# Kernel optimization log

Hardware: AMD Instinct MI355X
Metric: run time of the kernel (lower is better)

## Reference

```python
import jax, jax.numpy as jnp
import numpy as np

B, S, HID, H = 4, 2048, 1024, 16
D = HID // H  # dim per head


def setup_inputs() -> dict:
    key = jax.random.key(0)
    ks = jax.random.split(key, 7)
    inp = {
        "q": jax.random.normal(ks[0], (B, S, HID), dtype=jnp.float32),
        "k": jax.random.normal(ks[1], (B, S, HID), dtype=jnp.float32),
        "v": jax.random.normal(ks[2], (B, S, HID), dtype=jnp.float32),
        # Linear weights stored as (in, out); applied as x @ W. use_bias=False.
        "Wq": jax.random.normal(ks[3], (HID, HID), dtype=jnp.float32) * (1.0 / np.sqrt(HID)),
        "Wk": jax.random.normal(ks[4], (HID, HID), dtype=jnp.float32) * (1.0 / np.sqrt(HID)),
        "Wv": jax.random.normal(ks[5], (HID, HID), dtype=jnp.float32) * (1.0 / np.sqrt(HID)),
        "Wo": jax.random.normal(ks[6], (HID, HID), dtype=jnp.float32) * (1.0 / np.sqrt(HID)),
    }
    return inp


def reference(q, k, v, Wq, Wk, Wv, Wo):
    scale = 1.0 / jnp.sqrt(jnp.float32(D))
    # QKV projections, then split hidden into (H, D) heads (same layout as transpose_qkv)
    Q = (q @ Wq).reshape(B, S, H, D)
    K = (k @ Wk).reshape(B, S, H, D)
    V = (v @ Wv).reshape(B, S, H, D)
    # scaled dot-product attention: full [B,H,S,S] score matrix, softmax over keys
    attn_w = jnp.einsum("bqhd,bkhd->bhqk", Q, K) * scale
    attn_w = jax.nn.softmax(attn_w, axis=-1)
    # dropout rate is 0 (eval-mode / deterministic)
    O = jnp.einsum("bhqk,bkhd->bqhd", attn_w, V).reshape(B, S, HID)
    return O @ Wo
```

## Files before the change

### kernel.cpp

```cpp
#include <hip/hip_runtime.h>


typedef __attribute__((ext_vector_type(8))) short short8;
typedef __attribute__((ext_vector_type(4))) float float4v;

#if __has_builtin(__builtin_amdgcn_exp2f)
#define EXP2F(x) __builtin_amdgcn_exp2f(x)
#else
#define EXP2F(x) exp2f(x)
#endif

__device__ __forceinline__ unsigned short f2b(float x) {
  return (unsigned short)((__float_as_uint(x) + 0x8000u) >> 16);
}
__device__ __forceinline__ unsigned pk2f(float a, float b) {
  unsigned ua = __float_as_uint(a) + 0x8000u;
  unsigned ub = __float_as_uint(b) + 0x8000u;
  return __builtin_amdgcn_perm(ub, ua, 0x07060302);
}

typedef __attribute__((address_space(3))) unsigned int lds_uint;
typedef const __attribute__((address_space(1))) unsigned int gbl_uint;
__device__ __forceinline__ void stage16(const unsigned short* g, unsigned short* l) {
#if __has_builtin(__builtin_amdgcn_global_load_lds)
  __builtin_amdgcn_global_load_lds((gbl_uint*)g, (lds_uint*)l, 16, 0, 0);
#else
  *(uint4*)l = *(const uint4*)g;
#endif
}

__global__ __launch_bounds__(256) void conv_qkv(const float* __restrict__ q,
                                                const float* __restrict__ k,
                                                const float* __restrict__ v,
                                                unsigned short* __restrict__ ws,
                                                float qscale) {
  const int z = blockIdx.y;
  const float* src = z == 0 ? q : (z == 1 ? k : v);
  unsigned short* dst = ws + (size_t)z * 8388608;
  const float s = z == 0 ? qscale : 1.0f;
  size_t i = ((size_t)blockIdx.x * 256 + threadIdx.x) * 8;
  float4v a = *(const float4v*)(src + i);
  float4v b = *(const float4v*)(src + i + 4);
  uint4 o;
  o.x = pk2f(a.x * s, a.y * s);
  o.y = pk2f(a.z * s, a.w * s);
  o.z = pk2f(b.x * s, b.y * s);
  o.w = pk2f(b.z * s, b.w * s);
  *(uint4*)(dst + i) = o;
}

__global__ __launch_bounds__(256) void wtrans(const float* __restrict__ Wq,
                                              const float* __restrict__ Wk,
                                              const float* __restrict__ Wv,
                                              const float* __restrict__ Wo,
                                              unsigned short* __restrict__ Wt) {
  __shared__ float tile[32][33];
  const float* W = blockIdx.z == 0 ? Wq : blockIdx.z == 1 ? Wk
                   : blockIdx.z == 2 ? Wv : Wo;
  unsigned short* T = Wt + (size_t)blockIdx.z * 1048576;
  const int tx = threadIdx.x & 31, ty = threadIdx.x >> 5;
  const int k0 = blockIdx.y * 32, n0 = blockIdx.x * 32;
#pragma unroll
  for (int i = 0; i < 4; i++)
    tile[ty + 8 * i][tx] = W[(size_t)(k0 + ty + 8 * i) * 1024 + n0 + tx];
  __syncthreads();
#pragma unroll
  for (int i = 0; i < 4; i++)
    T[(size_t)(n0 + ty + 8 * i) * 1024 + k0 + tx] = f2b(tile[tx][ty + 8 * i]);
}

template <int MODE, bool SWAP>
__global__ __launch_bounds__(256, 2) void gemm_bt(const unsigned short* __restrict__ A,
                                                  const unsigned short* __restrict__ Bt,
                                                  void* __restrict__ Cg) {
  __shared__ __align__(16) unsigned short As[128 * 64];
  __shared__ __align__(16) unsigned short Bs[128 * 64];
  const int tid = threadIdx.x;
  const int lane = tid & 63;
  const int w = tid >> 6;
  const int quad = lane >> 4, col = lane & 15;
  const int wm = w >> 1, wn = w & 1;
  const int m0 = blockIdx.y * 128;
  const int n0 = blockIdx.x * 128;
  const int rA = lane >> 3, cA = lane & 7;

  float4v acc[4][4] = {};

  for (int k0 = 0; k0 < 1024; k0 += 64) {
    __syncthreads();
#pragma unroll
    for (int j = 0; j < 4; j++) {
      const int row = w * 32 + j * 8 + rA;
      stage16(A + (unsigned)(m0 + row) * 1024 + k0 + ((cA ^ rA) * 8),
              &As[row * 64 + cA * 8]);
      stage16(Bt + (unsigned)(n0 + row) * 1024 + k0 + ((cA ^ rA) * 8),
              &Bs[row * 64 + cA * 8]);
    }
    __syncthreads();

#pragma unroll
    for (int ks = 0; ks < 2; ks++) {
      short8 af[4], bf[4];
#pragma unroll
      for (int mi = 0; mi < 4; mi++) {
        int row = wm * 64 + mi * 16 + col;
        af[mi] = *(const short8*)&As[row * 64 + (((ks * 4 + quad) ^ (col & 7)) * 8)];
      }
#pragma unroll
      for (int ni = 0; ni < 4; ni++) {
        int row = wn * 64 + ni * 16 + col;
        bf[ni] = *(const short8*)&Bs[row * 64 + (((ks * 4 + quad) ^ (col & 7)) * 8)];
      }
#pragma unroll
      for (int mi = 0; mi < 4; mi++)
#pragma unroll
        for (int ni = 0; ni < 4; ni++) {
          if (SWAP)
            acc[ni][mi] = __builtin_amdgcn_mfma_f32_16x16x32_bf16(
                bf[ni], af[mi], acc[ni][mi], 0, 0, 0);
          else
            acc[mi][ni] = __builtin_amdgcn_mfma_f32_16x16x32_bf16(
                af[mi], bf[ni], acc[mi][ni], 0, 0, 0);
        }
    }
  }

  if (MODE == 0) {
#pragma unroll
    for (int ni = 0; ni < 4; ni++) {
      const int cg = n0 + wn * 64 + ni * 16 + quad * 4;
      const int h = cg >> 6, dlo = cg & 63;
#pragma unroll
      for (int mi = 0; mi < 4; mi++) {
        const int tok = m0 + wm * 64 + mi * 16 + col;
        const int b = tok >> 11, s = tok & 2047;
        uint2 pk;
        pk.x = pk2f(acc[ni][mi][0], acc[ni][mi][1]);
        pk.y = pk2f(acc[ni][mi][2], acc[ni][mi][3]);
        *(uint2*)((unsigned short*)Cg +
                  ((unsigned)((b * 16 + h) * 2048 + s) * 64 + dlo)) = pk;
      }
    }
  } else if (MODE == 1) {
#pragma unroll
    for (int mi = 0; mi < 4; mi++) {
      const int tok = m0 + wm * 64 + mi * 16 + quad * 4;
      const int b = tok >> 11, s = tok & 2047;
#pragma unroll
      for (int ni = 0; ni < 4; ni++) {
        const int cg = n0 + wn * 64 + ni * 16 + col;
        const int h = cg >> 6, d = cg & 63;
        uint2 pk;
        pk.x = pk2f(acc[mi][ni][0], acc[mi][ni][1]);
        pk.y = pk2f(acc[mi][ni][2], acc[mi][ni][3]);
        *(uint2*)((unsigned short*)Cg +
                  ((unsigned)((b * 16 + h) * 64 + d) * 2048 + s)) = pk;
      }
    }
  } else {
#pragma unroll
    for (int mi = 0; mi < 4; mi++) {
      const int row = m0 + wm * 64 + mi * 16 + quad * 4;
#pragma unroll
      for (int ni = 0; ni < 4; ni++) {
        const int cg = n0 + wn * 64 + ni * 16 + col;
#pragma unroll
        for (int r = 0; r < 4; r++)
          ((float*)Cg)[(unsigned)(row + r) * 1024 + cg] = acc[mi][ni][r];
      }
    }
  }
}

__global__ __launch_bounds__(256, 2) void attn_kernel(
    const unsigned short* __restrict__ Qb, const unsigned short* __restrict__ Kb,
    const unsigned short* __restrict__ Vt, unsigned short* __restrict__ Ob) {
  __shared__ __align__(16) unsigned short K_lds[128 * 64];
  __shared__ __align__(16) unsigned short V_lds[64 * 128];
  __shared__ __align__(16) unsigned short P_lds[128 * 128];
  __shared__ float den_lds[128];

  const int tid = threadIdx.x;
  const int lane = tid & 63;
  const int w = tid >> 6;
  const int quad = lane >> 4, col = lane & 15;
  const int wq = w >> 1, wk = w & 1;
  const int bh = blockIdx.y;
  const int qt = blockIdx.x;

  const unsigned short* Kbase = Kb + (size_t)bh * (2048 * 64);
  const unsigned short* Vbase = Vt + (size_t)bh * (64 * 2048);

  short8 qf[4][2];
#pragma unroll
  for (int qi = 0; qi < 4; qi++)
#pragma unroll
    for (int ks = 0; ks < 2; ks++) {
      int s = qt * 128 + wq * 64 + qi * 16 + col;
      qf[qi][ks] = *(const short8*)(Qb + ((size_t)bh * 2048 + s) * 64 + ks * 32 + quad * 8);
    }

  float4v oacc[2][4] = {};
  float dens[4] = {};

  if (tid < 128) den_lds[tid] = 0.f;

  const int rK = lane >> 3, cK = lane & 7;
  const int rV = lane >> 4, cV = lane & 15;

  for (int kt = 0; kt < 16; kt++) {
    const int s0 = kt * 128;
    __syncthreads();
#pragma unroll
    for (int j = 0; j < 4; j++) {
      const int rowK = w * 32 + j * 8 + rK;
      stage16(Kbase + (unsigned)(s0 + rowK) * 64 + ((cK ^ rK) * 8),
              &K_lds[rowK * 64 + cK * 8]);
      const int rowV = w * 16 + j * 4 + rV;
      stage16(Vbase + (unsigned)rowV * 2048 + s0 + (((cV ^ (rowV & 15)) & 15) * 8),
              &V_lds[rowV * 128 + cV * 8]);
    }
    __syncthreads();

    float4v sacc[4][4] = {};
    short8 kf[4][2];
#pragma unroll
    for (int ki = 0; ki < 4; ki++)
#pragma unroll
      for (int ks = 0; ks < 2; ks++) {
        int row = wk * 64 + ki * 16 + col;
        kf[ki][ks] = *(const short8*)&K_lds[row * 64 +
                                            (((ks * 4 + quad) ^ (col & 7)) * 8)];
      }
#pragma unroll
    for (int ki = 0; ki < 4; ki++)
#pragma unroll
      for (int qi = 0; qi < 4; qi++)
#pragma unroll
        for (int ks = 0; ks < 2; ks++)
          sacc[ki][qi] = __builtin_amdgcn_mfma_f32_16x16x32_bf16(
              kf[ki][ks], qf[qi][ks], sacc[ki][qi], 0, 0, 0);

#pragma unroll
    for (int ki = 0; ki < 4; ki++) {
      const int c = wk * 8 + ki * 2 + (quad >> 1);
      const int hh = quad & 1;
#pragma unroll
      for (int qi = 0; qi < 4; qi++) {
        const int q = wq * 64 + qi * 16 + col;
        float p0 = EXP2F(sacc[ki][qi][0]);
        float p1 = EXP2F(sacc[ki][qi][1]);
        float p2 = EXP2F(sacc[ki][qi][2]);
        float p3 = EXP2F(sacc[ki][qi][3]);
        dens[qi] += (p0 + p1) + (p2 + p3);
        uint2 pk;
        pk.x = pk2f(p0, p1);
        pk.y = pk2f(p2, p3);
        *(uint2*)&P_lds[q * 128 + ((c ^ col) & 15) * 8 + hh * 4] = pk;
      }
    }
    __syncthreads();

#pragma unroll
    for (int ks = 0; ks < 4; ks++) {
      short8 pf[4], vf[2];
#pragma unroll
      for (int mi = 0; mi < 4; mi++) {
        int row = wq * 64 + mi * 16 + col;
        pf[mi] = *(const short8*)&P_lds[row * 128 + ((((ks * 4 + quad) ^ col) & 15) * 8)];
      }
#pragma unroll
      for (int nv = 0; nv < 2; nv++) {
        int row = wk * 32 + nv * 16 + col;
        vf[nv] = *(const short8*)&V_lds[row * 128 + ((((ks * 4 + quad) ^ col) & 15) * 8)];
      }
#pragma unroll
      for (int nv = 0; nv < 2; nv++)
#pragma unroll
        for (int mi = 0; mi < 4; mi++)
          oacc[nv][mi] = __builtin_amdgcn_mfma_f32_16x16x32_bf16(
              vf[nv], pf[mi], oacc[nv][mi], 0, 0, 0);
    }
  }

#pragma unroll
  for (int qi = 0; qi < 4; qi++) {
    float v = dens[qi];
    v += __shfl_xor(v, 16);
    v += __shfl_xor(v, 32);
    if (lane < 16) atomicAdd(&den_lds[wq * 64 + qi * 16 + col], v);
  }
  __syncthreads();

  const int b = bh >> 4, h = bh & 15;
#pragma unroll
  for (int mi = 0; mi < 4; mi++) {
    const int srow = qt * 128 + wq * 64 + mi * 16 + col;
    const float rd = 1.f / den_lds[wq * 64 + mi * 16 + col];
    unsigned base = (unsigned)(b * 2048 + srow) * 1024 + h * 64;
#pragma unroll
    for (int nv = 0; nv < 2; nv++) {
      const int d0 = wk * 32 + nv * 16 + quad * 4;
      uint2 pk;
      pk.x = pk2f(oacc[nv][mi][0] * rd, oacc[nv][mi][1] * rd);
      pk.y = pk2f(oacc[nv][mi][2] * rd, oacc[nv][mi][3] * rd);
      *(uint2*)(Ob + base + d0) = pk;
    }
  }
}

extern "C" void kernel_launch(void* const* d_in, const int* in_sizes, int n_in,
                              void* d_out, int out_size, void* d_ws, size_t ws_size,
                              hipStream_t stream) {
  const float* q = (const float*)d_in[0];
  const float* k = (const float*)d_in[1];
  const float* v = (const float*)d_in[2];
  const float* Wq = (const float*)d_in[3];
  const float* Wk = (const float*)d_in[4];
  const float* Wv = (const float*)d_in[5];
  const float* Wo = (const float*)d_in[6];

  unsigned short* ws = (unsigned short*)d_ws;
  unsigned short* qb = ws;
  unsigned short* kb = ws + 8388608;
  unsigned short* vb = ws + 16777216;
  unsigned short* Qb = ws + 25165824;
  unsigned short* Kb = ws + 33554432;
  unsigned short* Vt = ws + 41943040;
  unsigned short* Wt = ws + 50331648;

  dim3 blk(256);
  const float qscale = 0.18033688011112042f;

  conv_qkv<<<dim3(4096, 3), blk, 0, stream>>>(q, k, v, ws, qscale);
  wtrans<<<dim3(32, 32, 4), blk, 0, stream>>>(Wq, Wk, Wv, Wo, Wt);

  dim3 gp(8, 64);
  gemm_bt<0, true><<<gp, blk, 0, stream>>>(qb, Wt + 0 * 1048576, Qb);
  gemm_bt<0, true><<<gp, blk, 0, stream>>>(kb, Wt + 1 * 1048576, Kb);
  gemm_bt<1, false><<<gp, blk, 0, stream>>>(vb, Wt + 2 * 1048576, Vt);

  attn_kernel<<<dim3(16, 64), blk, 0, stream>>>(Qb, Kb, Vt, qb );

  gemm_bt<2, false><<<gp, blk, 0, stream>>>(qb , Wt + 3 * 1048576, (float*)d_out);
}
```

Measured before the change: 356.2 us.

## Remap block indices for XCD-aware L2 locality and pad P tile stride

Switches the GEMM and attention launches to 1D grids and remaps block IDs so that blocks dispatched round-robin across the 8 XCDs share the same rows or heads within one XCD's L2. In the attention kernel, all q-tiles of a given head now tend to sit on the same XCD, so K/V reuse happens in L2. Separately, the P tile row stride in LDS is padded from 128 to 160 elements to change the bank mapping. The padding raises LDS use per block, which could reduce occupancy.

```diff
diff --git a/kernel.cpp b/kernel.cpp
--- a/kernel.cpp
+++ b/kernel.cpp
@@ -80,8 +80,10 @@
   const int w = tid >> 6;
   const int quad = lane >> 4, col = lane & 15;
   const int wm = w >> 1, wn = w & 1;
-  const int m0 = blockIdx.y * 128;
-  const int n0 = blockIdx.x * 128;
+  const int lin = blockIdx.x;
+  const int xcd = lin & 7, grp = lin >> 3;
+  const int m0 = ((grp & 7) * 8 + xcd) * 128;
+  const int n0 = (grp >> 3) * 128;
   const int rA = lane >> 3, cA = lane & 7;
 
   float4v acc[4][4] = {};
@@ -172,12 +174,13 @@
   }
 }
 
+#define PSTR 160
 __global__ __launch_bounds__(256, 2) void attn_kernel(
     const unsigned short* __restrict__ Qb, const unsigned short* __restrict__ Kb,
     const unsigned short* __restrict__ Vt, unsigned short* __restrict__ Ob) {
   __shared__ __align__(16) unsigned short K_lds[128 * 64];
   __shared__ __align__(16) unsigned short V_lds[64 * 128];
-  __shared__ __align__(16) unsigned short P_lds[128 * 128];
+  __shared__ __align__(16) unsigned short P_lds[128 * PSTR];
   __shared__ float den_lds[128];
 
   const int tid = threadIdx.x;
@@ -185,8 +188,9 @@
   const int w = tid >> 6;
   const int quad = lane >> 4, col = lane & 15;
   const int wq = w >> 1, wk = w & 1;
-  const int bh = blockIdx.y;
-  const int qt = blockIdx.x;
+  const int lin = blockIdx.x;
+  const int bh = ((lin >> 3) & 7) * 8 + (lin & 7);
+  const int qt = lin >> 6;
 
   const unsigned short* Kbase = Kb + (size_t)bh * (2048 * 64);
   const unsigned short* Vbase = Vt + (size_t)bh * (64 * 2048);
@@ -256,7 +260,7 @@
         uint2 pk;
         pk.x = pk2f(p0, p1);
         pk.y = pk2f(p2, p3);
-        *(uint2*)&P_lds[q * 128 + ((c ^ col) & 15) * 8 + hh * 4] = pk;
+        *(uint2*)&P_lds[q * PSTR + ((c ^ col) & 15) * 8 + hh * 4] = pk;
       }
     }
     __syncthreads();
@@ -267,7 +271,7 @@
 #pragma unroll
       for (int mi = 0; mi < 4; mi++) {
         int row = wq * 64 + mi * 16 + col;
-        pf[mi] = *(const short8*)&P_lds[row * 128 + ((((ks * 4 + quad) ^ col) & 15) * 8)];
+        pf[mi] = *(const short8*)&P_lds[row * PSTR + ((((ks * 4 + quad) ^ col) & 15) * 8)];
       }
 #pragma unroll
       for (int nv = 0; nv < 2; nv++) {
@@ -335,12 +339,12 @@
   conv_qkv<<<dim3(4096, 3), blk, 0, stream>>>(q, k, v, ws, qscale);
   wtrans<<<dim3(32, 32, 4), blk, 0, stream>>>(Wq, Wk, Wv, Wo, Wt);
 
-  dim3 gp(8, 64);
-  gemm_bt<0, true><<<gp, blk, 0, stream>>>(qb, Wt + 0 * 1048576, Qb);
-  gemm_bt<0, true><<<gp, blk, 0, stream>>>(kb, Wt + 1 * 1048576, Kb);
-  gemm_bt<1, false><<<gp, blk, 0, stream>>>(vb, Wt + 2 * 1048576, Vt);
-
-  attn_kernel<<<dim3(16, 64), blk, 0, stream>>>(Qb, Kb, Vt, qb );
-
-  gemm_bt<2, false><<<gp, blk, 0, stream>>>(qb , Wt + 3 * 1048576, (float*)d_out);
-}
+  gemm_bt<0, true><<<dim3(512), blk, 0, stream>>>(qb, Wt + 0 * 1048576, Qb);
+  gemm_bt<0, true><<<dim3(512), blk, 0, stream>>>(kb, Wt + 1 * 1048576, Kb);
+  gemm_bt<1, false><<<dim3(512), blk, 0, stream>>>(vb, Wt + 2 * 1048576, Vt);
+
+  attn_kernel<<<dim3(1024), blk, 0, stream>>>(Qb, Kb, Vt, qb );
+
+  gemm_bt<2, false><<<dim3(512), blk, 0, stream>>>(qb , Wt + 3 * 1048576,
+                                                   (float*)d_out);
+}
```

Measured after the change: 350.4 us. Within noise of the previous version (-1.6%).
